# Kernel tuning notes

Hardware: AMD Instinct MI355X
Metric: run time of the kernel (lower is better)

Reference implementation:

```python
import jax, jax.numpy as jnp
import numpy as np

N_ENT = 14951   # entities (FB15K-style multimodal KG)
N_REL = 1345    # relations == number of context sub-graphs
N_NODES = 120000  # nodes in the batched context graph (b_x length)
N_EDGES = 480000  # edges in the normalized batched adjacency


def _glorot(key, shape):
    scale = np.sqrt(2.0 / (shape[0] + shape[1])).astype(np.float32)
    return jax.random.normal(key, shape, dtype=jnp.float32) * scale


def setup_inputs() -> dict:
    key = jax.random.key(0)
    ks = jax.random.split(key, 16)
    inp = {}
    inp["img_feat"] = jax.random.normal(ks[0], (N_ENT, 4096), dtype=jnp.float32)
    inp["text_feat"] = jax.random.normal(ks[1], (N_ENT, 300), dtype=jnp.float32)
    inp["rel_emb"] = jax.random.normal(ks[2], (N_REL, 300), dtype=jnp.float32)
    # learned parameters (eval mode: dropout = identity)
    inp["W_img_text"] = _glorot(ks[3], (4396, 100)); inp["b_img_text"] = jnp.zeros((100,), jnp.float32)
    inp["W_rel_input"] = _glorot(ks[4], (300, 100)); inp["b_rel_input"] = jnp.zeros((100,), jnp.float32)
    inp["W_gc1"] = _glorot(ks[5], (200, 256)); inp["b_gc1"] = jnp.zeros((256,), jnp.float32)
    inp["W_gc2"] = _glorot(ks[6], (256, 200)); inp["b_gc2"] = jnp.zeros((200,), jnp.float32)
    inp["W_emb"] = _glorot(ks[7], (400, 1)); inp["b_emb"] = jnp.zeros((1,), jnp.float32)
    inp["W_emb_out"] = _glorot(ks[8], (400, 200)); inp["b_emb_out"] = jnp.zeros((200,), jnp.float32)
    inp["W_rel"] = _glorot(ks[9], (300, 200)); inp["b_rel"] = jnp.zeros((200,), jnp.float32)
    # row-normalized adjacency of the batched context graph, as edge list
    inp["edge_weight"] = jax.random.uniform(ks[10], (N_EDGES,), dtype=jnp.float32)
    inp["b_x"] = jax.random.randint(ks[11], (N_NODES,), 0, N_ENT)
    inp["b_graph"] = jax.random.randint(ks[12], (N_NODES,), 0, N_REL)
    inp["edge_src"] = jax.random.randint(ks[13], (N_EDGES,), 0, N_NODES)
    inp["edge_dst"] = jax.random.randint(ks[14], (N_EDGES,), 0, N_NODES)
    return inp


def reference(img_feat, text_feat, rel_emb, W_img_text, b_img_text, W_rel_input,
              b_rel_input, W_gc1, b_gc1, W_gc2, b_gc2, W_emb, b_emb, W_emb_out,
              b_emb_out, W_rel, b_rel, edge_weight, b_x, b_graph, edge_src, edge_dst):
    seg_sum = lambda v, idx, n: jax.ops.segment_sum(v, idx, num_segments=n)

    def spmm(h):  # normalized adjacency @ h via edge-list gather/scatter
        return seg_sum(h[edge_src] * edge_weight[:, None], edge_dst, N_NODES)

    # multimodal entity encoder: Linear(4396 -> 100)
    emf = jnp.concatenate([img_feat, text_feat], axis=1) @ W_img_text + b_img_text
    # relation context encoder: Linear(300 -> 100) + ReLU
    rel_in = jax.nn.relu(rel_emb @ W_rel_input + b_rel_input)
    # batched context-graph node features [M, 200]
    h = jnp.concatenate([emf[b_x], rel_in[b_graph]], axis=1)
    # two-layer GCN encoder (SGCN1)
    h1 = jax.nn.relu(spmm(h @ W_gc1) + b_gc1)
    h2 = spmm(h1 @ W_gc2) + b_gc2          # [M, 200]
    # scatter_mean over entity ids, broadcast back
    cnt = seg_sum(jnp.ones((N_NODES,), h2.dtype), b_x, N_ENT)
    mean = seg_sum(h2, b_x, N_ENT) / jnp.maximum(cnt, 1.0)[:, None]
    emb = jnp.concatenate([h2, mean[b_x]], axis=1)   # [M, 400]
    score = emb @ W_emb + b_emb                      # [M, 1]
    # scatter_softmax over segments b_x (numerically stable)
    smax = jax.ops.segment_max(score, b_x, num_segments=N_ENT)
    e = jnp.exp(score - smax[b_x])
    z_s = e / seg_sum(e, b_x, N_ENT)[b_x]
    new_out = seg_sum(z_s * emb, b_x, N_ENT) @ W_emb_out + b_emb_out  # [N_ENT, 200]
    # relation output encoder: Linear(300 -> 200) + ReLU
    rel_context = jax.nn.relu(rel_emb @ W_rel + b_rel)                # [N_REL, 200]
    return new_out, rel_context
```

## Files before the change

kernel.cpp:

```cpp
#include <hip/hip_runtime.h>

#define N_ENT 14951
#define N_REL 1345
#define NNODE 120000
#define NEDGE 480000
#define MP_ENC 14976
#define KP_ENC 4480
#define NP_ENC 112
#define MROWS1 16320
#define NB_E 118
#define NB_N 15

static inline int ceil_div(int a, int b){ return (a + b - 1) / b; }

typedef __bf16 bf16x8 __attribute__((ext_vector_type(8)));
typedef float f32x4 __attribute__((ext_vector_type(4)));

__device__ inline unsigned short f2bf(float f){
  unsigned u = __float_as_uint(f);
  return (unsigned short)((u + 0x7fffu + ((u >> 16) & 1u)) >> 16);
}
__device__ inline float bf2f(unsigned short b){
  return __uint_as_float(((unsigned)b) << 16);
}

__global__ __launch_bounds__(256) void enc_mfma(
    const float* __restrict__ img, const float* __restrict__ txt,
    const unsigned short* __restrict__ Wt1, float* __restrict__ part)
{
  __shared__ unsigned short As[64 * 40];
  __shared__ unsigned short Bs[112 * 40];
  const int t = threadIdx.x;
  const int m0 = blockIdx.x * 64;
  const int s = blockIdx.y;
  const int l = t & 63, w = t >> 6;
  f32x4 acc[7];
  #pragma unroll
  for (int i = 0; i < 7; i++) acc[i] = f32x4{0.f, 0.f, 0.f, 0.f};

  for (int step = 0; step < 35; ++step) {
    const int kb = s * 1120 + step * 32;
    #pragma unroll
    for (int p = 0; p < 2; ++p) {
      const int c = t + p * 256;
      const int row = c >> 3, kq = c & 7;
      const int rowg = m0 + row;
      const int k = kb + kq * 4;
      float4 v = make_float4(0.f, 0.f, 0.f, 0.f);
      if (rowg < N_ENT) {
        if (k < 4096)      v = *(const float4*)(img + (size_t)rowg * 4096 + k);
        else if (k < 4396) v = *(const float4*)(txt + (size_t)rowg * 300 + (k - 4096));
      }
      ushort4 b;
      b.x = f2bf(v.x); b.y = f2bf(v.y); b.z = f2bf(v.z); b.w = f2bf(v.w);
      *(ushort4*)&As[row * 40 + kq * 4] = b;
    }
    {
      const int n = t >> 2, k16 = t & 3;
      *(uint4*)&Bs[n * 40 + k16 * 8] = *(const uint4*)(Wt1 + (size_t)n * KP_ENC + kb + k16 * 8);
      if (t < 192) {
        const int c = t + 256;
        const int n2 = c >> 2, k2 = c & 3;
        *(uint4*)&Bs[n2 * 40 + k2 * 8] = *(const uint4*)(Wt1 + (size_t)n2 * KP_ENC + kb + k2 * 8);
      }
    }
    __syncthreads();
    bf16x8 a = *(const bf16x8*)&As[(w * 16 + (l & 15)) * 40 + (l >> 4) * 8];
    #pragma unroll
    for (int ct = 0; ct < 7; ++ct) {
      bf16x8 bb = *(const bf16x8*)&Bs[(ct * 16 + (l & 15)) * 40 + (l >> 4) * 8];
      acc[ct] = __builtin_amdgcn_mfma_f32_16x16x32_bf16(a, bb, acc[ct], 0, 0, 0);
    }
    __syncthreads();
  }
  const int rb = m0 + w * 16 + (l >> 4) * 4;
  const int col = l & 15;
  #pragma unroll
  for (int ct = 0; ct < 7; ++ct)
    #pragma unroll
    for (int i = 0; i < 4; ++i)
      part[((size_t)s * MP_ENC + rb + i) * NP_ENC + ct * 16 + col] = acc[ct][i];
}

__global__ __launch_bounds__(256) void enc_reduce(
    const float* __restrict__ part, const float* __restrict__ bias,
    unsigned short* __restrict__ feat1)
{
  int i = blockIdx.x * 256 + threadIdx.x;
  if (i >= N_ENT * 100) return;
  int r = i / 100, c = i % 100;
  float v = bias[c];
  #pragma unroll
  for (int s = 0; s < 4; ++s) v += part[((size_t)s * MP_ENC + r) * NP_ENC + c];
  feat1[(size_t)r * 224 + c] = f2bf(v);
}

__global__ __launch_bounds__(256) void rin_pack(
    const float* __restrict__ rin, unsigned short* __restrict__ feat1)
{
  int i = blockIdx.x * 256 + threadIdx.x;
  if (i >= N_REL * 100) return;
  int r = i / 100, c = i % 100;
  feat1[(size_t)(N_ENT + r) * 224 + 100 + c] = f2bf(rin[i]);
}

__global__ __launch_bounds__(256) void egr1_mfma(
    const unsigned short* __restrict__ feat1, const unsigned short* __restrict__ Wtg1,
    unsigned short* __restrict__ egr1)
{
  __shared__ unsigned short As[64 * 40];
  __shared__ unsigned short Bs[256 * 40];
  const int t = threadIdx.x;
  const int m0 = blockIdx.x * 64;
  const int l = t & 63, w = t >> 6;
  f32x4 acc[16];
  #pragma unroll
  for (int i = 0; i < 16; i++) acc[i] = f32x4{0.f, 0.f, 0.f, 0.f};

  for (int step = 0; step < 7; ++step) {
    const int kb = step * 32;
    {
      const int row = t >> 2, kc = t & 3;
      *(uint4*)&As[row * 40 + kc * 8] = *(const uint4*)(feat1 + (size_t)(m0 + row) * 224 + kb + kc * 8);
    }
    #pragma unroll
    for (int p = 0; p < 4; ++p) {
      const int c = t + p * 256;
      const int n = c >> 2, k16 = c & 3;
      *(uint4*)&Bs[n * 40 + k16 * 8] = *(const uint4*)(Wtg1 + (size_t)n * 224 + kb + k16 * 8);
    }
    __syncthreads();
    bf16x8 a = *(const bf16x8*)&As[(w * 16 + (l & 15)) * 40 + (l >> 4) * 8];
    #pragma unroll
    for (int ct = 0; ct < 16; ++ct) {
      bf16x8 bb = *(const bf16x8*)&Bs[(ct * 16 + (l & 15)) * 40 + (l >> 4) * 8];
      acc[ct] = __builtin_amdgcn_mfma_f32_16x16x32_bf16(a, bb, acc[ct], 0, 0, 0);
    }
    __syncthreads();
  }
  const int rb = m0 + w * 16 + (l >> 4) * 4;
  const int col0 = l & 15;
  #pragma unroll
  for (int ct = 0; ct < 16; ++ct) {
    const int col = ct * 16 + col0;
    #pragma unroll
    for (int i = 0; i < 4; ++i)
      egr1[(size_t)(rb + i) * 256 + col] = f2bf(acc[ct][i]);
  }
}

__global__ __launch_bounds__(256) void gemm2_mfma(
    const unsigned short* __restrict__ h1, const unsigned short* __restrict__ Wt2,
    unsigned short* __restrict__ hg2)
{
  __shared__ unsigned short As[64 * 40];
  __shared__ unsigned short Bs[208 * 40];
  const int t = threadIdx.x;
  const int m0 = blockIdx.x * 64;
  const int l = t & 63, w = t >> 6;
  f32x4 acc[13];
  #pragma unroll
  for (int i = 0; i < 13; i++) acc[i] = f32x4{0.f, 0.f, 0.f, 0.f};

  for (int step = 0; step < 8; ++step) {
    const int kb = step * 32;
    {
      const int row = t >> 2, kc = t & 3;
      *(uint4*)&As[row * 40 + kc * 8] = *(const uint4*)(h1 + (size_t)(m0 + row) * 256 + kb + kc * 8);
    }
    #pragma unroll
    for (int p = 0; p < 4; ++p) {
      const int c = t + p * 256;
      if (c < 832) {
        const int n = c >> 2, k16 = c & 3;
        *(uint4*)&Bs[n * 40 + k16 * 8] = *(const uint4*)(Wt2 + (size_t)n * 256 + kb + k16 * 8);
      }
    }
    __syncthreads();
    bf16x8 a = *(const bf16x8*)&As[(w * 16 + (l & 15)) * 40 + (l >> 4) * 8];
    #pragma unroll
    for (int ct = 0; ct < 13; ++ct) {
      bf16x8 bb = *(const bf16x8*)&Bs[(ct * 16 + (l & 15)) * 40 + (l >> 4) * 8];
      acc[ct] = __builtin_amdgcn_mfma_f32_16x16x32_bf16(a, bb, acc[ct], 0, 0, 0);
    }
    __syncthreads();
  }
  const int rb = m0 + w * 16 + (l >> 4) * 4;
  const int col0 = l & 15;
  #pragma unroll
  for (int ct = 0; ct < 13; ++ct) {
    const int col = ct * 16 + col0;
    #pragma unroll
    for (int i = 0; i < 4; ++i)
      hg2[(size_t)(rb + i) * 208 + col] = f2bf(acc[ct][i]);
  }
}

__global__ __launch_bounds__(256) void fin_mfma(
    const unsigned short* __restrict__ embA, const unsigned short* __restrict__ Wteo,
    const float* __restrict__ b_eo, float* __restrict__ out)
{
  __shared__ unsigned short As[64 * 40];
  __shared__ unsigned short Bs[208 * 40];
  const int t = threadIdx.x;
  const int m0 = blockIdx.x * 64;
  const int l = t & 63, w = t >> 6;
  f32x4 acc[13];
  #pragma unroll
  for (int i = 0; i < 13; i++) acc[i] = f32x4{0.f, 0.f, 0.f, 0.f};

  for (int step = 0; step < 13; ++step) {
    const int kb = step * 32;
    {
      const int row = t >> 2, kc = t & 3;
      *(uint4*)&As[row * 40 + kc * 8] = *(const uint4*)(embA + (size_t)(m0 + row) * 416 + kb + kc * 8);
    }
    #pragma unroll
    for (int p = 0; p < 4; ++p) {
      const int c = t + p * 256;
      if (c < 832) {
        const int n = c >> 2, k16 = c & 3;
        *(uint4*)&Bs[n * 40 + k16 * 8] = *(const uint4*)(Wteo + (size_t)n * 416 + kb + k16 * 8);
      }
    }
    __syncthreads();
    bf16x8 a = *(const bf16x8*)&As[(w * 16 + (l & 15)) * 40 + (l >> 4) * 8];
    #pragma unroll
    for (int ct = 0; ct < 13; ++ct) {
      bf16x8 bb = *(const bf16x8*)&Bs[(ct * 16 + (l & 15)) * 40 + (l >> 4) * 8];
      acc[ct] = __builtin_amdgcn_mfma_f32_16x16x32_bf16(a, bb, acc[ct], 0, 0, 0);
    }
    __syncthreads();
  }
  const int rb = m0 + w * 16 + (l >> 4) * 4;
  const int col0 = l & 15;
  #pragma unroll
  for (int ct = 0; ct < 13; ++ct) {
    const int col = ct * 16 + col0;
    if (col < 200) {
      const float b = b_eo[col];
      #pragma unroll
      for (int i = 0; i < 4; ++i) {
        const int r = rb + i;
        if (r < N_ENT) out[(size_t)r * 200 + col] = acc[ct][i] + b;
      }
    }
  }
}

__global__ __launch_bounds__(256) void wt_all_k(
    const float* __restrict__ W_it, const float* __restrict__ W_g1,
    const float* __restrict__ W_g2, const float* __restrict__ W_eo,
    unsigned short* __restrict__ Wt1, unsigned short* __restrict__ Wtg1,
    unsigned short* __restrict__ Wt2, unsigned short* __restrict__ Wteo)
{
  int i = blockIdx.x * 256 + threadIdx.x;
  if (i < NP_ENC * KP_ENC) {
    int n = i / KP_ENC, k = i % KP_ENC;
    float v = (n < 100 && k < 4396) ? W_it[(size_t)k * 100 + n] : 0.f;
    Wt1[i] = f2bf(v);
    return;
  }
  i -= NP_ENC * KP_ENC;
  if (i < 256 * 224) {
    int n = i / 224, k = i % 224;
    float v = (k < 200) ? W_g1[(size_t)k * 256 + n] : 0.f;
    Wtg1[i] = f2bf(v);
    return;
  }
  i -= 256 * 224;
  if (i < 208 * 256) {
    int n = i >> 8, k = i & 255;
    float v = (n < 200) ? W_g2[(size_t)k * 200 + n] : 0.f;
    Wt2[i] = f2bf(v);
    return;
  }
  i -= 208 * 256;
  if (i < 208 * 416) {
    int n = i / 416, k = i % 416;
    float v = (n < 200 && k < 400) ? W_eo[(size_t)k * 200 + n] : 0.f;
    Wteo[i] = f2bf(v);
  }
}

template<bool RELU, bool HASBIAS>
__global__ __launch_bounds__(256) void gemm_f32(
    const float* __restrict__ A1, int K1, const float* __restrict__ A2,
    const float* __restrict__ B, const float* __restrict__ bias,
    float* __restrict__ C, int M, int K, int N)
{
  constexpr int BM = 64, BN = 128, BK = 16;
  __shared__ float As[BK][BM + 4];
  __shared__ float Bs[BK][BN];
  const int t = threadIdx.x;
  const int m0 = blockIdx.y * BM, n0 = blockIdx.x * BN;
  const int tr = t >> 4, tc = t & 15;
  const int tm0 = tr * 4, tn0 = tc * 8;
  const int K2 = K - K1;
  const int arow = t >> 2, aq = (t & 3) * 4;
  const int brow = t >> 4, bc0 = (t & 15) * 4;
  float acc[4][8];
  #pragma unroll
  for (int i = 0; i < 4; i++)
    #pragma unroll
    for (int j = 0; j < 8; j++) acc[i][j] = 0.f;

  for (int k0 = 0; k0 < K; k0 += BK) {
    {
      const int r = m0 + arow;
      const int k = k0 + aq;
      float4 v = make_float4(0.f, 0.f, 0.f, 0.f);
      if (r < M) {
        if (k + 3 < K1) {
          v = *(const float4*)(A1 + (size_t)r * K1 + k);
        } else if (k >= K1 && (k - K1) + 3 < K2) {
          v = *(const float4*)(A2 + (size_t)r * K2 + (k - K1));
        } else {
          float tmp[4] = {0.f, 0.f, 0.f, 0.f};
          #pragma unroll
          for (int j = 0; j < 4; j++) {
            int kj = k + j;
            if (kj < K) tmp[j] = (kj < K1) ? A1[(size_t)r * K1 + kj]
                                           : A2[(size_t)r * K2 + (kj - K1)];
          }
          v = make_float4(tmp[0], tmp[1], tmp[2], tmp[3]);
        }
// ... 112 lines not shown
    __syncthreads();
    s[t] += u;
    __syncthreads();
  }
  if (t < nb) partial[t] = s[t] - v;
  if (t == 255) *(eregion ? ebase_end : nbase_end) = s[255];
}

#define NB3_E 469
__global__ __launch_bounds__(256) void scan3_k(
    int* __restrict__ ebase, const int* __restrict__ epart,
    int* __restrict__ nbase, const int* __restrict__ npart)
{
  if (blockIdx.x < NB3_E) {
    int i = blockIdx.x * 256 + threadIdx.x;
    if (i < NNODE) ebase[i] += epart[i >> 10];
  } else {
    int i = (blockIdx.x - NB3_E) * 256 + threadIdx.x;
    if (i < N_ENT) nbase[i] += npart[i >> 10];
  }
}

__global__ __launch_bounds__(256) void scatter2_k(
    const int* __restrict__ esrc, const int* __restrict__ edst, const float* __restrict__ ew,
    const int* __restrict__ bx, const int* __restrict__ bg,
    const int* __restrict__ ebase, int* __restrict__ ecur,
    float* __restrict__ s_w, int* __restrict__ s_src,
    int* __restrict__ s_en, int* __restrict__ s_gn,
    const int* __restrict__ nbase, int* __restrict__ ncur, int* __restrict__ node_of)
{
  int i = blockIdx.x * 256 + threadIdx.x;
  if (i < NEDGE) {
    int d = edst[i];
    int p = ebase[d] + atomicAdd(&ecur[d], 1);
    int s = esrc[i];
    s_w[p] = ew[i];
    s_src[p] = s;
    s_en[p] = bx[s];
    s_gn[p] = bg[s];
    return;
  }
  i -= NEDGE;
  if (i < NNODE) {
    int ent = bx[i];
    int p = nbase[ent] + atomicAdd(&ncur[ent], 1);
    node_of[p] = i;
  }
}

__global__ __launch_bounds__(256) void spmm1_g(
    const int* __restrict__ ebase, const float* __restrict__ s_w,
    const int* __restrict__ s_en, const int* __restrict__ s_gn,
    const unsigned short* __restrict__ egr1,
    const float* __restrict__ b_g1, unsigned short* __restrict__ h1)
{
  const int gid = blockIdx.x * blockDim.x + threadIdx.x;
  const int d = gid >> 6, lane = gid & 63;
  if (d >= NNODE) return;
  const int p0 = ebase[d], p1 = ebase[d + 1];
  float acc[4] = {0.f, 0.f, 0.f, 0.f};
  for (int p = p0; p < p1; ++p) {
    const float w = s_w[p];
    const int en = s_en[p], gn = s_gn[p];
    const ushort4 va = *(const ushort4*)(egr1 + (size_t)en * 256 + lane * 4);
    const ushort4 vb = *(const ushort4*)(egr1 + (size_t)(N_ENT + gn) * 256 + lane * 4);
    acc[0] += w * (bf2f(va.x) + bf2f(vb.x));
    acc[1] += w * (bf2f(va.y) + bf2f(vb.y));
    acc[2] += w * (bf2f(va.z) + bf2f(vb.z));
    acc[3] += w * (bf2f(va.w) + bf2f(vb.w));
  }
  const float4 b = ((const float4*)b_g1)[lane];
  ushort4 o;
  o.x = f2bf(fmaxf(acc[0] + b.x, 0.f));
  o.y = f2bf(fmaxf(acc[1] + b.y, 0.f));
  o.z = f2bf(fmaxf(acc[2] + b.z, 0.f));
  o.w = f2bf(fmaxf(acc[3] + b.w, 0.f));
  *(ushort4*)(h1 + (size_t)d * 256 + lane * 4) = o;
}

__global__ __launch_bounds__(256) void spmm2_g(
    const int* __restrict__ ebase, const float* __restrict__ s_w,
    const int* __restrict__ s_src, const unsigned short* __restrict__ hg2,
    const float* __restrict__ b_g2, const float* __restrict__ W_e,
    float* __restrict__ h2, float* __restrict__ score)
{
  const int gid = blockIdx.x * blockDim.x + threadIdx.x;
  const int d = gid >> 6, lane = gid & 63;
  if (d >= NNODE) return;
  const int p0 = ebase[d], p1 = ebase[d + 1];
  float acc[4] = {0.f, 0.f, 0.f, 0.f};
  const int col = lane * 4;
  if (lane < 52) {
    for (int p = p0; p < p1; ++p) {
      const float w = s_w[p];
      const ushort4 v = *(const ushort4*)(hg2 + (size_t)s_src[p] * 208 + col);
      acc[0] += w * bf2f(v.x); acc[1] += w * bf2f(v.y);
      acc[2] += w * bf2f(v.z); acc[3] += w * bf2f(v.w);
    }
  }
  float sp = 0.f;
  if (col < 200) {
    const float4 b = ((const float4*)b_g2)[lane];
    acc[0] += b.x; acc[1] += b.y; acc[2] += b.z; acc[3] += b.w;
    *(float4*)(h2 + (size_t)d * 200 + col) = make_float4(acc[0], acc[1], acc[2], acc[3]);
    const float4 we = ((const float4*)W_e)[lane];
    sp = acc[0] * we.x + acc[1] * we.y + acc[2] * we.z + acc[3] * we.w;
  }
  #pragma unroll
  for (int off = 32; off; off >>= 1) sp += __shfl_xor(sp, off);
  if (lane == 0) score[d] = sp;
}

__global__ __launch_bounds__(256) void ent_k(
    const int* __restrict__ nbase, const int* __restrict__ node_of,
    const float* __restrict__ h2, const float* __restrict__ score,
    unsigned short* __restrict__ embA)
{
  const int gid = blockIdx.x * blockDim.x + threadIdx.x;
  const int ent = gid >> 6, lane = gid & 63;
  if (ent >= N_ENT) return;
  const int p0 = nbase[ent], p1 = nbase[ent + 1];
  const int cnt = p1 - p0;
  float m = -3.4e38f;
  for (int p = p0 + lane; p < p1; p += 64) m = fmaxf(m, score[node_of[p]]);
  #pragma unroll
  for (int off = 32; off; off >>= 1) m = fmaxf(m, __shfl_xor(m, off));
  float es = 0.f;
  for (int p = p0 + lane; p < p1; p += 64) es += __expf(score[node_of[p]] - m);
  #pragma unroll
  for (int off = 32; off; off >>= 1) es += __shfl_xor(es, off);
  const float inv_es = (cnt > 0) ? 1.f / es : 0.f;
  const float inv_cnt = 1.f / fmaxf((float)cnt, 1.f);
  float4 aw = make_float4(0.f, 0.f, 0.f, 0.f);
  float4 am = make_float4(0.f, 0.f, 0.f, 0.f);
  for (int p = p0; p < p1; ++p) {
    const int nd = node_of[p];
    const float z = __expf(score[nd] - m) * inv_es;
    if (lane < 50) {
      const float4 v = ((const float4*)(h2 + (size_t)nd * 200))[lane];
      aw.x += z * v.x; aw.y += z * v.y; aw.z += z * v.z; aw.w += z * v.w;
      am.x += v.x; am.y += v.y; am.z += v.z; am.w += v.w;
    }
  }
  if (lane < 50) {
    ushort4 ow, om;
    ow.x = f2bf(aw.x); ow.y = f2bf(aw.y); ow.z = f2bf(aw.z); ow.w = f2bf(aw.w);
    om.x = f2bf(am.x * inv_cnt); om.y = f2bf(am.y * inv_cnt);
    om.z = f2bf(am.z * inv_cnt); om.w = f2bf(am.w * inv_cnt);
    *(ushort4*)(embA + (size_t)ent * 416 + lane * 4) = ow;
    *(ushort4*)(embA + (size_t)ent * 416 + 200 + lane * 4) = om;
  }
}

extern "C" void kernel_launch(void* const* d_in, const int* in_sizes, int n_in,
                              void* d_out, int out_size, void* d_ws, size_t ws_size,
                              hipStream_t stream)
{
  const float* img  = (const float*)d_in[0];
  const float* txt  = (const float*)d_in[1];
  const float* rel  = (const float*)d_in[2];
  const float* W_it = (const float*)d_in[3];
  const float* b_it = (const float*)d_in[4];
  const float* W_ri = (const float*)d_in[5];
  const float* b_ri = (const float*)d_in[6];
  const float* W_g1 = (const float*)d_in[7];
  const float* b_g1 = (const float*)d_in[8];
  const float* W_g2 = (const float*)d_in[9];
  const float* b_g2 = (const float*)d_in[10];
  const float* W_e  = (const float*)d_in[11];
  const float* W_eo = (const float*)d_in[13];
  const float* b_eo = (const float*)d_in[14];
  const float* W_r  = (const float*)d_in[15];
  const float* b_r  = (const float*)d_in[16];
  const float* ew   = (const float*)d_in[17];
  const int*   bx   = (const int*)d_in[18];
  const int*   bg   = (const int*)d_in[19];
  const int*   esrc = (const int*)d_in[20];
  const int*   edst = (const int*)d_in[21];

  float* ws = (float*)d_ws;
  size_t off = 0;
  auto alloc = [&](size_t n){ size_t r = off; off += (n + 255) & ~(size_t)255; return r; };
  unsigned short* feat1 = (unsigned short*)(ws + alloc((size_t)MROWS1 * 224 / 2));
  unsigned short* egr1  = (unsigned short*)(ws + alloc((size_t)MROWS1 * 256 / 2));
  unsigned short* h1    = (unsigned short*)(ws + alloc((size_t)NNODE * 256 / 2));
  unsigned short* hg2   = (unsigned short*)(ws + alloc((size_t)NNODE * 208 / 2));
  unsigned short* embA  = (unsigned short*)(ws + alloc((size_t)MP_ENC * 416 / 2));
  float* h2    = ws + alloc((size_t)NNODE * 200);
  float* rin   = ws + alloc((size_t)N_REL * 100);
  float* score = ws + alloc(NNODE);
  size_t cnt0 = alloc((size_t)NNODE * 2 + (size_t)N_ENT * 2);
  int* ehist = (int*)(ws + cnt0);
  int* ecur  = ehist + NNODE;
  int* nhist = ecur + NNODE;
  int* ncur  = nhist + N_ENT;
  int* ebase = (int*)(ws + alloc(NNODE + 1));
  int* nbase = (int*)(ws + alloc(N_ENT + 1));
  int* epart = (int*)(ws + alloc(256));
  int* npart = (int*)(ws + alloc(256));
  float* s_w  = ws + alloc(NEDGE);
  int* s_src  = (int*)(ws + alloc(NEDGE));
  int* s_en   = (int*)(ws + alloc(NEDGE));
  int* s_gn   = (int*)(ws + alloc(NEDGE));
  int* node_of = (int*)(ws + alloc(NNODE));
  unsigned short* Wt1  = (unsigned short*)(ws + alloc((size_t)NP_ENC * KP_ENC / 2));
  unsigned short* Wtg1 = (unsigned short*)(ws + alloc((size_t)256 * 224 / 2));
  unsigned short* Wt2  = (unsigned short*)(ws + alloc((size_t)208 * 256 / 2));
  unsigned short* Wteo = (unsigned short*)(ws + alloc((size_t)208 * 416 / 2));
  float* part = h2;

  dim3 blk(256);

  hipMemsetAsync(ehist, 0, ((size_t)NNODE * 2 + (size_t)N_ENT * 2) * 4, stream);
  hipMemsetAsync(feat1, 0, (size_t)MROWS1 * 224 * 2, stream);
  hipMemsetAsync(embA,  0, (size_t)MP_ENC * 416 * 2, stream);

  hist2_k<<<ceil_div(NEDGE + NNODE, 256), blk, 0, stream>>>(edst, bx, ehist, nhist);
  scan1_k<<<NB_E + NB_N, blk, 0, stream>>>(ehist, ebase, epart, nhist, nbase, npart);
  scan2_k<<<2, blk, 0, stream>>>(epart, ebase + NNODE, npart, nbase + N_ENT);
  scan3_k<<<NB3_E + ceil_div(N_ENT, 256), blk, 0, stream>>>(ebase, epart, nbase, npart);
  scatter2_k<<<ceil_div(NEDGE + NNODE, 256), blk, 0, stream>>>(
      esrc, edst, ew, bx, bg, ebase, ecur, s_w, s_src, s_en, s_gn, nbase, ncur, node_of);

  wt_all_k<<<ceil_div(NP_ENC * KP_ENC + 256 * 224 + 208 * 256 + 208 * 416, 256), blk, 0, stream>>>(
      W_it, W_g1, W_g2, W_eo, Wt1, Wtg1, Wt2, Wteo);

  enc_mfma<<<dim3(MP_ENC / 64, 4), blk, 0, stream>>>(img, txt, Wt1, part);
  enc_reduce<<<ceil_div(N_ENT * 100, 256), blk, 0, stream>>>(part, b_it, feat1);
  gemm_f32<true, true><<<dim3(1, ceil_div(N_REL, 64)), blk, 0, stream>>>(
      rel, 300, rel, W_ri, b_ri, rin, N_REL, 300, 100);
  rin_pack<<<ceil_div(N_REL * 100, 256), blk, 0, stream>>>(rin, feat1);

  egr1_mfma<<<MROWS1 / 64, blk, 0, stream>>>(feat1, Wtg1, egr1);
  spmm1_g<<<ceil_div(NNODE * 64, 256), blk, 0, stream>>>(
      ebase, s_w, s_en, s_gn, egr1, b_g1, h1);

  gemm2_mfma<<<NNODE / 64, blk, 0, stream>>>(h1, Wt2, hg2);
  spmm2_g<<<ceil_div(NNODE * 64, 256), blk, 0, stream>>>(
      ebase, s_w, s_src, hg2, b_g2, W_e, h2, score);

  ent_k<<<ceil_div(N_ENT * 64, 256), blk, 0, stream>>>(nbase, node_of, h2, score, embA);

  float* out_new = (float*)d_out;
  float* out_rel = out_new + (size_t)N_ENT * 200;
  fin_mfma<<<MP_ENC / 64, blk, 0, stream>>>(embA, Wteo, b_eo, out_new);
  gemm_f32<true, true><<<dim3(2, ceil_div(N_REL, 64)), blk, 0, stream>>>(
      rel, 300, rel, W_r, b_r, out_rel, N_REL, 300, 200);
}
```

Baseline: 618.1 us.

## Register-prefetch MFMA GEMM tiles, widen encoder split-K, store h2 in bf16

Each MFMA GEMM kernel (encoder, GCN layer 1, layer 2, final) now loads the next K-slice from global memory into registers while the current slice is consumed from LDS. This hides global load latency behind the MFMA work. The encoder split-K grows from 4 to 8 slices (K padded to 4608) to put more blocks on the device, at the cost of a larger partial buffer and a longer reduction. h2 is stored as bf16 instead of fp32 to halve the traffic of the gather in ent_k, which lowers precision and needs its own buffer instead of aliasing the partials.

Result: slower. 719.8 us (+16.5%).

```diff
diff --git a/kernel.cpp b/kernel.cpp
--- a/kernel.cpp
+++ b/kernel.cpp
@@ -5,8 +5,11 @@
 #define NNODE 120000
 #define NEDGE 480000
 #define MP_ENC 14976
-#define KP_ENC 4480
+#define KP_ENC 4608
 #define NP_ENC 112
+#define ENC_SPLIT 8
+#define ENC_KSPLIT 576
+#define ENC_STEPS 18
 #define MROWS1 16320
 #define NB_E 118
 #define NB_N 15
@@ -38,8 +41,8 @@
   #pragma unroll
   for (int i = 0; i < 7; i++) acc[i] = f32x4{0.f, 0.f, 0.f, 0.f};
 
-  for (int step = 0; step < 35; ++step) {
-    const int kb = s * 1120 + step * 32;
+  auto loadA = [&](int step, float4* va) {
+    const int kb = s * ENC_KSPLIT + step * 32;
     #pragma unroll
     for (int p = 0; p < 2; ++p) {
       const int c = t + p * 256;
@@ -51,20 +54,39 @@
         if (k < 4096)      v = *(const float4*)(img + (size_t)rowg * 4096 + k);
         else if (k < 4396) v = *(const float4*)(txt + (size_t)rowg * 300 + (k - 4096));
       }
+      va[p] = v;
+    }
+  };
+  auto loadB = [&](int step, uint4* vb) {
+    const int kb = s * ENC_KSPLIT + step * 32;
+    vb[0] = *(const uint4*)(Wt1 + (size_t)(t >> 2) * KP_ENC + kb + (t & 3) * 8);
+    if (t < 192) {
+      const int c = t + 256;
+      vb[1] = *(const uint4*)(Wt1 + (size_t)(c >> 2) * KP_ENC + kb + (c & 3) * 8);
+    }
+  };
+  auto storeAB = [&](const float4* va, const uint4* vb) {
+    #pragma unroll
+    for (int p = 0; p < 2; ++p) {
+      const int c = t + p * 256;
+      const int row = c >> 3, kq = c & 7;
       ushort4 b;
-      b.x = f2bf(v.x); b.y = f2bf(v.y); b.z = f2bf(v.z); b.w = f2bf(v.w);
+      b.x = f2bf(va[p].x); b.y = f2bf(va[p].y); b.z = f2bf(va[p].z); b.w = f2bf(va[p].w);
       *(ushort4*)&As[row * 40 + kq * 4] = b;
     }
-    {
-      const int n = t >> 2, k16 = t & 3;
-      *(uint4*)&Bs[n * 40 + k16 * 8] = *(const uint4*)(Wt1 + (size_t)n * KP_ENC + kb + k16 * 8);
-      if (t < 192) {
-        const int c = t + 256;
-        const int n2 = c >> 2, k2 = c & 3;
-        *(uint4*)&Bs[n2 * 40 + k2 * 8] = *(const uint4*)(Wt1 + (size_t)n2 * KP_ENC + kb + k2 * 8);
-      }
-    }
-    __syncthreads();
+    *(uint4*)&Bs[(t >> 2) * 40 + (t & 3) * 8] = vb[0];
+    if (t < 192) {
+      const int c = t + 256;
+      *(uint4*)&Bs[(c >> 2) * 40 + (c & 3) * 8] = vb[1];
+    }
+  };
+
+  float4 va[2]; uint4 vb[2];
+  loadA(0, va); loadB(0, vb);
+  for (int step = 0; step < ENC_STEPS; ++step) {
+    storeAB(va, vb);
+    __syncthreads();
+    if (step + 1 < ENC_STEPS) { loadA(step + 1, va); loadB(step + 1, vb); }
     bf16x8 a = *(const bf16x8*)&As[(w * 16 + (l & 15)) * 40 + (l >> 4) * 8];
     #pragma unroll
     for (int ct = 0; ct < 7; ++ct) {
@@ -91,7 +113,7 @@
   int r = i / 100, c = i % 100;
   float v = bias[c];
   #pragma unroll
-  for (int s = 0; s < 4; ++s) v += part[((size_t)s * MP_ENC + r) * NP_ENC + c];
+  for (int s = 0; s < ENC_SPLIT; ++s) v += part[((size_t)s * MP_ENC + r) * NP_ENC + c];
   feat1[(size_t)r * 224 + c] = f2bf(v);
 }
 
@@ -117,19 +139,30 @@
   #pragma unroll
   for (int i = 0; i < 16; i++) acc[i] = f32x4{0.f, 0.f, 0.f, 0.f};
 
-  for (int step = 0; step < 7; ++step) {
+  auto loadAB = [&](int step, uint4& pa, uint4* pb) {
     const int kb = step * 32;
-    {
-      const int row = t >> 2, kc = t & 3;
-      *(uint4*)&As[row * 40 + kc * 8] = *(const uint4*)(feat1 + (size_t)(m0 + row) * 224 + kb + kc * 8);
-    }
+    pa = *(const uint4*)(feat1 + (size_t)(m0 + (t >> 2)) * 224 + kb + (t & 3) * 8);
     #pragma unroll
     for (int p = 0; p < 4; ++p) {
       const int c = t + p * 256;
-      const int n = c >> 2, k16 = c & 3;
-      *(uint4*)&Bs[n * 40 + k16 * 8] = *(const uint4*)(Wtg1 + (size_t)n * 224 + kb + k16 * 8);
-    }
-    __syncthreads();
+      pb[p] = *(const uint4*)(Wtg1 + (size_t)(c >> 2) * 224 + kb + (c & 3) * 8);
+    }
+  };
+  auto storeAB = [&](const uint4& pa, const uint4* pb) {
+    *(uint4*)&As[(t >> 2) * 40 + (t & 3) * 8] = pa;
+    #pragma unroll
+    for (int p = 0; p < 4; ++p) {
+      const int c = t + p * 256;
+      *(uint4*)&Bs[(c >> 2) * 40 + (c & 3) * 8] = pb[p];
+    }
+  };
+
+  uint4 pa; uint4 pb[4];
+  loadAB(0, pa, pb);
+  for (int step = 0; step < 7; ++step) {
+    storeAB(pa, pb);
+    __syncthreads();
+    if (step + 1 < 7) loadAB(step + 1, pa, pb);
     bf16x8 a = *(const bf16x8*)&As[(w * 16 + (l & 15)) * 40 + (l >> 4) * 8];
     #pragma unroll
     for (int ct = 0; ct < 16; ++ct) {
@@ -162,21 +195,30 @@
   #pragma unroll
   for (int i = 0; i < 13; i++) acc[i] = f32x4{0.f, 0.f, 0.f, 0.f};
 
-  for (int step = 0; step < 8; ++step) {
+  auto loadAB = [&](int step, uint4& pa, uint4* pb) {
     const int kb = step * 32;
-    {
-      const int row = t >> 2, kc = t & 3;
-      *(uint4*)&As[row * 40 + kc * 8] = *(const uint4*)(h1 + (size_t)(m0 + row) * 256 + kb + kc * 8);
-    }
+    pa = *(const uint4*)(h1 + (size_t)(m0 + (t >> 2)) * 256 + kb + (t & 3) * 8);
     #pragma unroll
     for (int p = 0; p < 4; ++p) {
       const int c = t + p * 256;
-      if (c < 832) {
-        const int n = c >> 2, k16 = c & 3;
-        *(uint4*)&Bs[n * 40 + k16 * 8] = *(const uint4*)(Wt2 + (size_t)n * 256 + kb + k16 * 8);
-      }
-    }
-    __syncthreads();
+      if (c < 832) pb[p] = *(const uint4*)(Wt2 + (size_t)(c >> 2) * 256 + kb + (c & 3) * 8);
+    }
+  };
+  auto storeAB = [&](const uint4& pa, const uint4* pb) {
+    *(uint4*)&As[(t >> 2) * 40 + (t & 3) * 8] = pa;
+    #pragma unroll
+    for (int p = 0; p < 4; ++p) {
+      const int c = t + p * 256;
+      if (c < 832) *(uint4*)&Bs[(c >> 2) * 40 + (c & 3) * 8] = pb[p];
+    }
+  };
+
+  uint4 pa; uint4 pb[4];
+  loadAB(0, pa, pb);
+  for (int step = 0; step < 8; ++step) {
+    storeAB(pa, pb);
+    __syncthreads();
+    if (step + 1 < 8) loadAB(step + 1, pa, pb);
     bf16x8 a = *(const bf16x8*)&As[(w * 16 + (l & 15)) * 40 + (l >> 4) * 8];
     #pragma unroll
     for (int ct = 0; ct < 13; ++ct) {
@@ -209,21 +251,30 @@
   #pragma unroll
   for (int i = 0; i < 13; i++) acc[i] = f32x4{0.f, 0.f, 0.f, 0.f};
 
-  for (int step = 0; step < 13; ++step) {
+  auto loadAB = [&](int step, uint4& pa, uint4* pb) {
     const int kb = step * 32;
-    {
-      const int row = t >> 2, kc = t & 3;
-      *(uint4*)&As[row * 40 + kc * 8] = *(const uint4*)(embA + (size_t)(m0 + row) * 416 + kb + kc * 8);
-    }
+    pa = *(const uint4*)(embA + (size_t)(m0 + (t >> 2)) * 416 + kb + (t & 3) * 8);
     #pragma unroll
     for (int p = 0; p < 4; ++p) {
       const int c = t + p * 256;
-      if (c < 832) {
-        const int n = c >> 2, k16 = c & 3;
-        *(uint4*)&Bs[n * 40 + k16 * 8] = *(const uint4*)(Wteo + (size_t)n * 416 + kb + k16 * 8);
-      }
-    }
-    __syncthreads();
+      if (c < 832) pb[p] = *(const uint4*)(Wteo + (size_t)(c >> 2) * 416 + kb + (c & 3) * 8);
+    }
+  };
+  auto storeAB = [&](const uint4& pa, const uint4* pb) {
+    *(uint4*)&As[(t >> 2) * 40 + (t & 3) * 8] = pa;
+    #pragma unroll
+    for (int p = 0; p < 4; ++p) {
+      const int c = t + p * 256;
+      if (c < 832) *(uint4*)&Bs[(c >> 2) * 40 + (c & 3) * 8] = pb[p];
+    }
+  };
+
+  uint4 pa; uint4 pb[4];
+  loadAB(0, pa, pb);
+  for (int step = 0; step < 13; ++step) {
+    storeAB(pa, pb);
+    __syncthreads();
+    if (step + 1 < 13) loadAB(step + 1, pa, pb);
     bf16x8 a = *(const bf16x8*)&As[(w * 16 + (l & 15)) * 40 + (l >> 4) * 8];
     #pragma unroll
     for (int ct = 0; ct < 13; ++ct) {
@@ -520,7 +571,7 @@
     const int* __restrict__ ebase, const float* __restrict__ s_w,
     const int* __restrict__ s_src, const unsigned short* __restrict__ hg2,
     const float* __restrict__ b_g2, const float* __restrict__ W_e,
-    float* __restrict__ h2, float* __restrict__ score)
+    unsigned short* __restrict__ h2, float* __restrict__ score)
 {
   const int gid = blockIdx.x * blockDim.x + threadIdx.x;
   const int d = gid >> 6, lane = gid & 63;
@@ -528,19 +579,19 @@
   const int p0 = ebase[d], p1 = ebase[d + 1];
   float acc[4] = {0.f, 0.f, 0.f, 0.f};
   const int col = lane * 4;
-  if (lane < 52) {
+  float sp = 0.f;
+  if (lane < 50) {
     for (int p = p0; p < p1; ++p) {
       const float w = s_w[p];
       const ushort4 v = *(const ushort4*)(hg2 + (size_t)s_src[p] * 208 + col);
       acc[0] += w * bf2f(v.x); acc[1] += w * bf2f(v.y);
       acc[2] += w * bf2f(v.z); acc[3] += w * bf2f(v.w);
     }
-  }
-  float sp = 0.f;
-  if (col < 200) {
     const float4 b = ((const float4*)b_g2)[lane];
     acc[0] += b.x; acc[1] += b.y; acc[2] += b.z; acc[3] += b.w;
-    *(float4*)(h2 + (size_t)d * 200 + col) = make_float4(acc[0], acc[1], acc[2], acc[3]);
+    ushort4 o;
+    o.x = f2bf(acc[0]); o.y = f2bf(acc[1]); o.z = f2bf(acc[2]); o.w = f2bf(acc[3]);
+    *(ushort4*)(h2 + (size_t)d * 200 + col) = o;
     const float4 we = ((const float4*)W_e)[lane];
     sp = acc[0] * we.x + acc[1] * we.y + acc[2] * we.z + acc[3] * we.w;
   }
@@ -551,7 +602,7 @@
 
 __global__ __launch_bounds__(256) void ent_k(
     const int* __restrict__ nbase, const int* __restrict__ node_of,
-    const float* __restrict__ h2, const float* __restrict__ score,
+    const unsigned short* __restrict__ h2, const float* __restrict__ score,
     unsigned short* __restrict__ embA)
 {
   const int gid = blockIdx.x * blockDim.x + threadIdx.x;
@@ -569,22 +620,23 @@
   for (int off = 32; off; off >>= 1) es += __shfl_xor(es, off);
   const float inv_es = (cnt > 0) ? 1.f / es : 0.f;
   const float inv_cnt = 1.f / fmaxf((float)cnt, 1.f);
-  float4 aw = make_float4(0.f, 0.f, 0.f, 0.f);
-  float4 am = make_float4(0.f, 0.f, 0.f, 0.f);
+  float aw[4] = {0.f, 0.f, 0.f, 0.f};
+  float am[4] = {0.f, 0.f, 0.f, 0.f};
   for (int p = p0; p < p1; ++p) {
     const int nd = node_of[p];
     const float z = __expf(score[nd] - m) * inv_es;
     if (lane < 50) {
-      const float4 v = ((const float4*)(h2 + (size_t)nd * 200))[lane];
-      aw.x += z * v.x; aw.y += z * v.y; aw.z += z * v.z; aw.w += z * v.w;
-      am.x += v.x; am.y += v.y; am.z += v.z; am.w += v.w;
+      const ushort4 v = *(const ushort4*)(h2 + (size_t)nd * 200 + lane * 4);
+      const float vx = bf2f(v.x), vy = bf2f(v.y), vz = bf2f(v.z), vw = bf2f(v.w);
+      aw[0] += z * vx; aw[1] += z * vy; aw[2] += z * vz; aw[3] += z * vw;
+      am[0] += vx; am[1] += vy; am[2] += vz; am[3] += vw;
     }
   }
   if (lane < 50) {
     ushort4 ow, om;
-    ow.x = f2bf(aw.x); ow.y = f2bf(aw.y); ow.z = f2bf(aw.z); ow.w = f2bf(aw.w);
-    om.x = f2bf(am.x * inv_cnt); om.y = f2bf(am.y * inv_cnt);
-    om.z = f2bf(am.z * inv_cnt); om.w = f2bf(am.w * inv_cnt);
+    ow.x = f2bf(aw[0]); ow.y = f2bf(aw[1]); ow.z = f2bf(aw[2]); ow.w = f2bf(aw[3]);
+    om.x = f2bf(am[0] * inv_cnt); om.y = f2bf(am[1] * inv_cnt);
+    om.z = f2bf(am[2] * inv_cnt); om.w = f2bf(am[3] * inv_cnt);
     *(ushort4*)(embA + (size_t)ent * 416 + lane * 4) = ow;
     *(ushort4*)(embA + (size_t)ent * 416 + 200 + lane * 4) = om;
   }
@@ -624,7 +676,8 @@
   unsigned short* h1    = (unsigned short*)(ws + alloc((size_t)NNODE * 256 / 2));
   unsigned short* hg2   = (unsigned short*)(ws + alloc((size_t)NNODE * 208 / 2));
   unsigned short* embA  = (unsigned short*)(ws + alloc((size_t)MP_ENC * 416 / 2));
-  float* h2    = ws + alloc((size_t)NNODE * 200);
+  unsigned short* h2    = (unsigned short*)(ws + alloc((size_t)NNODE * 200 / 2));
+  float* part  = ws + alloc((size_t)ENC_SPLIT * MP_ENC * NP_ENC);
   float* rin   = ws + alloc((size_t)N_REL * 100);
   float* score = ws + alloc(NNODE);
   size_t cnt0 = alloc((size_t)NNODE * 2 + (size_t)N_ENT * 2);
@@ -645,7 +698,6 @@
   unsigned short* Wtg1 = (unsigned short*)(ws + alloc((size_t)256 * 224 / 2));
   unsigned short* Wt2  = (unsigned short*)(ws + alloc((size_t)208 * 256 / 2));
   unsigned short* Wteo = (unsigned short*)(ws + alloc((size_t)208 * 416 / 2));
-  float* part = h2;
 
   dim3 blk(256);
 
@@ -663,7 +715,7 @@
   wt_all_k<<<ceil_div(NP_ENC * KP_ENC + 256 * 224 + 208 * 256 + 208 * 416, 256), blk, 0, stream>>>(
       W_it, W_g1, W_g2, W_eo, Wt1, Wtg1, Wt2, Wteo);
 
-  enc_mfma<<<dim3(MP_ENC / 64, 4), blk, 0, stream>>>(img, txt, Wt1, part);
+  enc_mfma<<<dim3(MP_ENC / 64, ENC_SPLIT), blk, 0, stream>>>(img, txt, Wt1, part);
   enc_reduce<<<ceil_div(N_ENT * 100, 256), blk, 0, stream>>>(part, b_it, feat1);
   gemm_f32<true, true><<<dim3(1, ceil_div(N_REL, 64)), blk, 0, stream>>>(
       rel, 300, rel, W_ri, b_ri, rin, N_REL, 300, 100);
```

## Load MFMA operands directly from global, widen encoder split-K, store h2 as bf16

Applied to the files above, without the earlier changes.

The GEMM kernels stop staging tiles through LDS. Each lane now loads its A and B fragments straight from global memory in MFMA layout, which removes both __syncthreads per K step. The encoder GEMM doubles its split-K to 8 and pads K to 4608, giving more blocks to fill the GPU, at the cost of a bigger partial buffer and a longer reduction. h2 is stored as bf16 instead of fp32, which halves its write and gather traffic in spmm2 and ent_k but lowers precision. The risk is redundant, less-coalesced global loads of B across waves.

Result: slower. 772.7 us (+25.0%).

```diff
diff --git a/kernel.cpp b/kernel.cpp
--- a/kernel.cpp
+++ b/kernel.cpp
@@ -5,8 +5,11 @@
 #define NNODE 120000
 #define NEDGE 480000
 #define MP_ENC 14976
-#define KP_ENC 4480
+#define KP_ENC 4608
 #define NP_ENC 112
+#define ENC_SPLIT 8
+#define ENC_KSPLIT 576
+#define ENC_STEPS 18
 #define MROWS1 16320
 #define NB_E 118
 #define NB_N 15
@@ -15,6 +18,7 @@
 
 typedef __bf16 bf16x8 __attribute__((ext_vector_type(8)));
 typedef float f32x4 __attribute__((ext_vector_type(4)));
+union U8 { unsigned short u[8]; bf16x8 v; };
 
 __device__ inline unsigned short f2bf(float f){
   unsigned u = __float_as_uint(f);
@@ -28,58 +32,54 @@
     const float* __restrict__ img, const float* __restrict__ txt,
     const unsigned short* __restrict__ Wt1, float* __restrict__ part)
 {
-  __shared__ unsigned short As[64 * 40];
-  __shared__ unsigned short Bs[112 * 40];
   const int t = threadIdx.x;
-  const int m0 = blockIdx.x * 64;
+  const int w = t >> 6, l = t & 63;
   const int s = blockIdx.y;
-  const int l = t & 63, w = t >> 6;
+  const int row16 = blockIdx.x * 64 + w * 16;
+  int row = row16 + (l & 15);
+  if (row >= N_ENT) row = N_ENT - 1;
+  const int koff = (l >> 4) * 8;
   f32x4 acc[7];
   #pragma unroll
   for (int i = 0; i < 7; i++) acc[i] = f32x4{0.f, 0.f, 0.f, 0.f};
 
-  for (int step = 0; step < 35; ++step) {
-    const int kb = s * 1120 + step * 32;
-    #pragma unroll
-    for (int p = 0; p < 2; ++p) {
-      const int c = t + p * 256;
-      const int row = c >> 3, kq = c & 7;
-      const int rowg = m0 + row;
-      const int k = kb + kq * 4;
-      float4 v = make_float4(0.f, 0.f, 0.f, 0.f);
-      if (rowg < N_ENT) {
-        if (k < 4096)      v = *(const float4*)(img + (size_t)rowg * 4096 + k);
-        else if (k < 4396) v = *(const float4*)(txt + (size_t)rowg * 300 + (k - 4096));
+  const float* irow = img + (size_t)row * 4096;
+  const float* trow = txt + (size_t)row * 300;
+  const unsigned short* bcol = Wt1 + (size_t)(l & 15) * KP_ENC;
+
+  for (int step = 0; step < ENC_STEPS; ++step) {
+    const int c = s * ENC_KSPLIT + step * 32 + koff;
+    float4 u0 = make_float4(0.f, 0.f, 0.f, 0.f);
+    float4 u1 = make_float4(0.f, 0.f, 0.f, 0.f);
+    if (c + 8 <= 4096) {
+      u0 = *(const float4*)(irow + c);
+      u1 = *(const float4*)(irow + c + 4);
+    } else if (c >= 4096) {
+      const int ct_ = c - 4096;
+      if (ct_ <= 288) {
+        u0 = *(const float4*)(trow + ct_);
+        u1 = *(const float4*)(trow + ct_ + 4);
+      } else if (ct_ == 296) {
+        u0 = *(const float4*)(trow + 296);
       }
-      ushort4 b;
-      b.x = f2bf(v.x); b.y = f2bf(v.y); b.z = f2bf(v.z); b.w = f2bf(v.w);
-      *(ushort4*)&As[row * 40 + kq * 4] = b;
-    }
-    {
-      const int n = t >> 2, k16 = t & 3;
-      *(uint4*)&Bs[n * 40 + k16 * 8] = *(const uint4*)(Wt1 + (size_t)n * KP_ENC + kb + k16 * 8);
-      if (t < 192) {
-        const int c = t + 256;
-        const int n2 = c >> 2, k2 = c & 3;
-        *(uint4*)&Bs[n2 * 40 + k2 * 8] = *(const uint4*)(Wt1 + (size_t)n2 * KP_ENC + kb + k2 * 8);
-      }
-    }
-    __syncthreads();
-    bf16x8 a = *(const bf16x8*)&As[(w * 16 + (l & 15)) * 40 + (l >> 4) * 8];
+    }
+    U8 pa;
+    pa.u[0] = f2bf(u0.x); pa.u[1] = f2bf(u0.y); pa.u[2] = f2bf(u0.z); pa.u[3] = f2bf(u0.w);
+    pa.u[4] = f2bf(u1.x); pa.u[5] = f2bf(u1.y); pa.u[6] = f2bf(u1.z); pa.u[7] = f2bf(u1.w);
+    const bf16x8 a = pa.v;
     #pragma unroll
     for (int ct = 0; ct < 7; ++ct) {
-      bf16x8 bb = *(const bf16x8*)&Bs[(ct * 16 + (l & 15)) * 40 + (l >> 4) * 8];
-      acc[ct] = __builtin_amdgcn_mfma_f32_16x16x32_bf16(a, bb, acc[ct], 0, 0, 0);
-    }
-    __syncthreads();
-  }
-  const int rb = m0 + w * 16 + (l >> 4) * 4;
-  const int col = l & 15;
+      const bf16x8 b = *(const bf16x8*)(bcol + (size_t)ct * 16 * KP_ENC + c);
+      acc[ct] = __builtin_amdgcn_mfma_f32_16x16x32_bf16(a, b, acc[ct], 0, 0, 0);
+    }
+  }
+  const int orow = row16 + (koff >> 1);
+  float* pp = part + (size_t)s * MP_ENC * NP_ENC;
   #pragma unroll
   for (int ct = 0; ct < 7; ++ct)
     #pragma unroll
     for (int i = 0; i < 4; ++i)
-      part[((size_t)s * MP_ENC + rb + i) * NP_ENC + ct * 16 + col] = acc[ct][i];
+      pp[(size_t)(orow + i) * NP_ENC + ct * 16 + (l & 15)] = acc[ct][i];
 }
 
 __global__ __launch_bounds__(256) void enc_reduce(
@@ -91,7 +91,7 @@
   int r = i / 100, c = i % 100;
   float v = bias[c];
   #pragma unroll
-  for (int s = 0; s < 4; ++s) v += part[((size_t)s * MP_ENC + r) * NP_ENC + c];
+  for (int s = 0; s < ENC_SPLIT; ++s) v += part[((size_t)s * MP_ENC + r) * NP_ENC + c];
   feat1[(size_t)r * 224 + c] = f2bf(v);
 }
 
@@ -104,144 +104,83 @@
   feat1[(size_t)(N_ENT + r) * 224 + 100 + c] = f2bf(rin[i]);
 }
 
+template<int NT, int KSTEPS, int LDA, int LDB>
+__device__ inline void dgemm_body(
+    const unsigned short* __restrict__ A, const unsigned short* __restrict__ Wt,
+    int row16, int l, f32x4* acc)
+{
+  const int koff = (l >> 4) * 8;
+  const unsigned short* arow = A + (size_t)(row16 + (l & 15)) * LDA + koff;
+  const unsigned short* bcol = Wt + (size_t)(l & 15) * LDB + koff;
+  for (int step = 0; step < KSTEPS; ++step) {
+    const int k = step * 32;
+    const bf16x8 a = *(const bf16x8*)(arow + k);
+    #pragma unroll
+    for (int ct = 0; ct < NT; ++ct) {
+      const bf16x8 b = *(const bf16x8*)(bcol + (size_t)ct * 16 * LDB + k);
+      acc[ct] = __builtin_amdgcn_mfma_f32_16x16x32_bf16(a, b, acc[ct], 0, 0, 0);
+    }
+  }
+}
+
 __global__ __launch_bounds__(256) void egr1_mfma(
     const unsigned short* __restrict__ feat1, const unsigned short* __restrict__ Wtg1,
     unsigned short* __restrict__ egr1)
 {
-  __shared__ unsigned short As[64 * 40];
-  __shared__ unsigned short Bs[256 * 40];
   const int t = threadIdx.x;
-  const int m0 = blockIdx.x * 64;
-  const int l = t & 63, w = t >> 6;
+  const int w = t >> 6, l = t & 63;
+  const int row16 = blockIdx.x * 64 + w * 16;
   f32x4 acc[16];
   #pragma unroll
   for (int i = 0; i < 16; i++) acc[i] = f32x4{0.f, 0.f, 0.f, 0.f};
-
-  for (int step = 0; step < 7; ++step) {
-    const int kb = step * 32;
-    {
-      const int row = t >> 2, kc = t & 3;
-      *(uint4*)&As[row * 40 + kc * 8] = *(const uint4*)(feat1 + (size_t)(m0 + row) * 224 + kb + kc * 8);
-    }
-    #pragma unroll
-    for (int p = 0; p < 4; ++p) {
-      const int c = t + p * 256;
-      const int n = c >> 2, k16 = c & 3;
-      *(uint4*)&Bs[n * 40 + k16 * 8] = *(const uint4*)(Wtg1 + (size_t)n * 224 + kb + k16 * 8);
-    }
-    __syncthreads();
-    bf16x8 a = *(const bf16x8*)&As[(w * 16 + (l & 15)) * 40 + (l >> 4) * 8];
-    #pragma unroll
-    for (int ct = 0; ct < 16; ++ct) {
-      bf16x8 bb = *(const bf16x8*)&Bs[(ct * 16 + (l & 15)) * 40 + (l >> 4) * 8];
-      acc[ct] = __builtin_amdgcn_mfma_f32_16x16x32_bf16(a, bb, acc[ct], 0, 0, 0);
-    }
-    __syncthreads();
-  }
-  const int rb = m0 + w * 16 + (l >> 4) * 4;
-  const int col0 = l & 15;
-  #pragma unroll
-  for (int ct = 0; ct < 16; ++ct) {
-    const int col = ct * 16 + col0;
+  dgemm_body<16, 7, 224, 224>(feat1, Wtg1, row16, l, acc);
+  const int orow = row16 + ((l >> 4) << 2);
+  #pragma unroll
+  for (int ct = 0; ct < 16; ++ct)
     #pragma unroll
     for (int i = 0; i < 4; ++i)
-      egr1[(size_t)(rb + i) * 256 + col] = f2bf(acc[ct][i]);
-  }
+      egr1[(size_t)(orow + i) * 256 + ct * 16 + (l & 15)] = f2bf(acc[ct][i]);
 }
 
 __global__ __launch_bounds__(256) void gemm2_mfma(
     const unsigned short* __restrict__ h1, const unsigned short* __restrict__ Wt2,
     unsigned short* __restrict__ hg2)
 {
-  __shared__ unsigned short As[64 * 40];
-  __shared__ unsigned short Bs[208 * 40];
   const int t = threadIdx.x;
-  const int m0 = blockIdx.x * 64;
-  const int l = t & 63, w = t >> 6;
+  const int w = t >> 6, l = t & 63;
+  const int row16 = blockIdx.x * 64 + w * 16;
   f32x4 acc[13];
   #pragma unroll
   for (int i = 0; i < 13; i++) acc[i] = f32x4{0.f, 0.f, 0.f, 0.f};
-
-  for (int step = 0; step < 8; ++step) {
-    const int kb = step * 32;
-    {
-      const int row = t >> 2, kc = t & 3;
-      *(uint4*)&As[row * 40 + kc * 8] = *(const uint4*)(h1 + (size_t)(m0 + row) * 256 + kb + kc * 8);
-    }
-    #pragma unroll
-    for (int p = 0; p < 4; ++p) {
-      const int c = t + p * 256;
-      if (c < 832) {
-        const int n = c >> 2, k16 = c & 3;
-        *(uint4*)&Bs[n * 40 + k16 * 8] = *(const uint4*)(Wt2 + (size_t)n * 256 + kb + k16 * 8);
-      }
-    }
-    __syncthreads();
-    bf16x8 a = *(const bf16x8*)&As[(w * 16 + (l & 15)) * 40 + (l >> 4) * 8];
-    #pragma unroll
-    for (int ct = 0; ct < 13; ++ct) {
-      bf16x8 bb = *(const bf16x8*)&Bs[(ct * 16 + (l & 15)) * 40 + (l >> 4) * 8];
-      acc[ct] = __builtin_amdgcn_mfma_f32_16x16x32_bf16(a, bb, acc[ct], 0, 0, 0);
-    }
-    __syncthreads();
-  }
-  const int rb = m0 + w * 16 + (l >> 4) * 4;
-  const int col0 = l & 15;
-  #pragma unroll
-  for (int ct = 0; ct < 13; ++ct) {
-    const int col = ct * 16 + col0;
+  dgemm_body<13, 8, 256, 256>(h1, Wt2, row16, l, acc);
+  const int orow = row16 + ((l >> 4) << 2);
+  #pragma unroll
+  for (int ct = 0; ct < 13; ++ct)
     #pragma unroll
     for (int i = 0; i < 4; ++i)
-      hg2[(size_t)(rb + i) * 208 + col] = f2bf(acc[ct][i]);
-  }
+      hg2[(size_t)(orow + i) * 208 + ct * 16 + (l & 15)] = f2bf(acc[ct][i]);
 }
 
 __global__ __launch_bounds__(256) void fin_mfma(
     const unsigned short* __restrict__ embA, const unsigned short* __restrict__ Wteo,
     const float* __restrict__ b_eo, float* __restrict__ out)
 {
-  __shared__ unsigned short As[64 * 40];
-  __shared__ unsigned short Bs[208 * 40];
   const int t = threadIdx.x;
-  const int m0 = blockIdx.x * 64;
-  const int l = t & 63, w = t >> 6;
+  const int w = t >> 6, l = t & 63;
+  const int row16 = blockIdx.x * 64 + w * 16;
   f32x4 acc[13];
   #pragma unroll
   for (int i = 0; i < 13; i++) acc[i] = f32x4{0.f, 0.f, 0.f, 0.f};
-
-  for (int step = 0; step < 13; ++step) {
-    const int kb = step * 32;
-    {
-      const int row = t >> 2, kc = t & 3;
-      *(uint4*)&As[row * 40 + kc * 8] = *(const uint4*)(embA + (size_t)(m0 + row) * 416 + kb + kc * 8);
-    }
-    #pragma unroll
-    for (int p = 0; p < 4; ++p) {
-      const int c = t + p * 256;
-      if (c < 832) {
-        const int n = c >> 2, k16 = c & 3;
-        *(uint4*)&Bs[n * 40 + k16 * 8] = *(const uint4*)(Wteo + (size_t)n * 416 + kb + k16 * 8);
-      }
-    }
-    __syncthreads();
-    bf16x8 a = *(const bf16x8*)&As[(w * 16 + (l & 15)) * 40 + (l >> 4) * 8];
-    #pragma unroll
-    for (int ct = 0; ct < 13; ++ct) {
-      bf16x8 bb = *(const bf16x8*)&Bs[(ct * 16 + (l & 15)) * 40 + (l >> 4) * 8];
-      acc[ct] = __builtin_amdgcn_mfma_f32_16x16x32_bf16(a, bb, acc[ct], 0, 0, 0);
-    }
-    __syncthreads();
-  }
-  const int rb = m0 + w * 16 + (l >> 4) * 4;
-  const int col0 = l & 15;
+  dgemm_body<13, 13, 416, 416>(embA, Wteo, row16, l, acc);
+  const int orow = row16 + ((l >> 4) << 2);
   #pragma unroll
   for (int ct = 0; ct < 13; ++ct) {
-    const int col = ct * 16 + col0;
+    const int col = ct * 16 + (l & 15);
     if (col < 200) {
       const float b = b_eo[col];
       #pragma unroll
       for (int i = 0; i < 4; ++i) {
-        const int r = rb + i;
+        const int r = orow + i;
         if (r < N_ENT) out[(size_t)r * 200 + col] = acc[ct][i] + b;
       }
     }
@@ -520,7 +459,7 @@
     const int* __restrict__ ebase, const float* __restrict__ s_w,
     const int* __restrict__ s_src, const unsigned short* __restrict__ hg2,
     const float* __restrict__ b_g2, const float* __restrict__ W_e,
-    float* __restrict__ h2, float* __restrict__ score)
+    unsigned short* __restrict__ h2, float* __restrict__ score)
 {
   const int gid = blockIdx.x * blockDim.x + threadIdx.x;
   const int d = gid >> 6, lane = gid & 63;
@@ -528,19 +467,19 @@
   const int p0 = ebase[d], p1 = ebase[d + 1];
   float acc[4] = {0.f, 0.f, 0.f, 0.f};
   const int col = lane * 4;
-  if (lane < 52) {
+  float sp = 0.f;
+  if (lane < 50) {
     for (int p = p0; p < p1; ++p) {
       const float w = s_w[p];
       const ushort4 v = *(const ushort4*)(hg2 + (size_t)s_src[p] * 208 + col);
       acc[0] += w * bf2f(v.x); acc[1] += w * bf2f(v.y);
       acc[2] += w * bf2f(v.z); acc[3] += w * bf2f(v.w);
     }
-  }
-  float sp = 0.f;
-  if (col < 200) {
     const float4 b = ((const float4*)b_g2)[lane];
     acc[0] += b.x; acc[1] += b.y; acc[2] += b.z; acc[3] += b.w;
-    *(float4*)(h2 + (size_t)d * 200 + col) = make_float4(acc[0], acc[1], acc[2], acc[3]);
+    ushort4 o;
+    o.x = f2bf(acc[0]); o.y = f2bf(acc[1]); o.z = f2bf(acc[2]); o.w = f2bf(acc[3]);
+    *(ushort4*)(h2 + (size_t)d * 200 + col) = o;
     const float4 we = ((const float4*)W_e)[lane];
     sp = acc[0] * we.x + acc[1] * we.y + acc[2] * we.z + acc[3] * we.w;
   }
@@ -551,7 +490,7 @@
 
 __global__ __launch_bounds__(256) void ent_k(
     const int* __restrict__ nbase, const int* __restrict__ node_of,
-    const float* __restrict__ h2, const float* __restrict__ score,
+    const unsigned short* __restrict__ h2, const float* __restrict__ score,
     unsigned short* __restrict__ embA)
 {
   const int gid = blockIdx.x * blockDim.x + threadIdx.x;
@@ -569,22 +508,23 @@
   for (int off = 32; off; off >>= 1) es += __shfl_xor(es, off);
   const float inv_es = (cnt > 0) ? 1.f / es : 0.f;
   const float inv_cnt = 1.f / fmaxf((float)cnt, 1.f);
-  float4 aw = make_float4(0.f, 0.f, 0.f, 0.f);
-  float4 am = make_float4(0.f, 0.f, 0.f, 0.f);
+  float aw[4] = {0.f, 0.f, 0.f, 0.f};
+  float am[4] = {0.f, 0.f, 0.f, 0.f};
   for (int p = p0; p < p1; ++p) {
     const int nd = node_of[p];
     const float z = __expf(score[nd] - m) * inv_es;
     if (lane < 50) {
-      const float4 v = ((const float4*)(h2 + (size_t)nd * 200))[lane];
-      aw.x += z * v.x; aw.y += z * v.y; aw.z += z * v.z; aw.w += z * v.w;
-      am.x += v.x; am.y += v.y; am.z += v.z; am.w += v.w;
+      const ushort4 v = *(const ushort4*)(h2 + (size_t)nd * 200 + lane * 4);
+      const float vx = bf2f(v.x), vy = bf2f(v.y), vz = bf2f(v.z), vw = bf2f(v.w);
+      aw[0] += z * vx; aw[1] += z * vy; aw[2] += z * vz; aw[3] += z * vw;
+      am[0] += vx; am[1] += vy; am[2] += vz; am[3] += vw;
     }
   }
   if (lane < 50) {
     ushort4 ow, om;
-    ow.x = f2bf(aw.x); ow.y = f2bf(aw.y); ow.z = f2bf(aw.z); ow.w = f2bf(aw.w);
-    om.x = f2bf(am.x * inv_cnt); om.y = f2bf(am.y * inv_cnt);
-    om.z = f2bf(am.z * inv_cnt); om.w = f2bf(am.w * inv_cnt);
+    ow.x = f2bf(aw[0]); ow.y = f2bf(aw[1]); ow.z = f2bf(aw[2]); ow.w = f2bf(aw[3]);
+    om.x = f2bf(am[0] * inv_cnt); om.y = f2bf(am[1] * inv_cnt);
+    om.z = f2bf(am[2] * inv_cnt); om.w = f2bf(am[3] * inv_cnt);
     *(ushort4*)(embA + (size_t)ent * 416 + lane * 4) = ow;
     *(ushort4*)(embA + (size_t)ent * 416 + 200 + lane * 4) = om;
   }
@@ -624,7 +564,8 @@
   unsigned short* h1    = (unsigned short*)(ws + alloc((size_t)NNODE * 256 / 2));
   unsigned short* hg2   = (unsigned short*)(ws + alloc((size_t)NNODE * 208 / 2));
   unsigned short* embA  = (unsigned short*)(ws + alloc((size_t)MP_ENC * 416 / 2));
-  float* h2    = ws + alloc((size_t)NNODE * 200);
+  unsigned short* h2    = (unsigned short*)(ws + alloc((size_t)NNODE * 200 / 2));
+  float* part  = ws + alloc((size_t)ENC_SPLIT * MP_ENC * NP_ENC);
   float* rin   = ws + alloc((size_t)N_REL * 100);
   float* score = ws + alloc(NNODE);
   size_t cnt0 = alloc((size_t)NNODE * 2 + (size_t)N_ENT * 2);
@@ -645,7 +586,6 @@
   unsigned short* Wtg1 = (unsigned short*)(ws + alloc((size_t)256 * 224 / 2));
   unsigned short* Wt2  = (unsigned short*)(ws + alloc((size_t)208 * 256 / 2));
   unsigned short* Wteo = (unsigned short*)(ws + alloc((size_t)208 * 416 / 2));
-  float* part = h2;
 
   dim3 blk(256);
 
@@ -663,7 +603,7 @@
   wt_all_k<<<ceil_div(NP_ENC * KP_ENC + 256 * 224 + 208 * 256 + 208 * 416, 256), blk, 0, stream>>>(
       W_it, W_g1, W_g2, W_eo, Wt1, Wtg1, Wt2, Wteo);
 
-  enc_mfma<<<dim3(MP_ENC / 64, 4), blk, 0, stream>>>(img, txt, Wt1, part);
+  enc_mfma<<<dim3(MP_ENC / 64, ENC_SPLIT), blk, 0, stream>>>(img, txt, Wt1, part);
   enc_reduce<<<ceil_div(N_ENT * 100, 256), blk, 0, stream>>>(part, b_it, feat1);
   gemm_f32<true, true><<<dim3(1, ceil_div(N_REL, 64)), blk, 0, stream>>>(
       rel, 300, rel, W_ri, b_ri, rin, N_REL, 300, 100);
```
